# Performance work log

Measured on AMD Instinct MI355X. Metric: run time of the kernel, lower is better.

## Reference

```python
import jax, jax.numpy as jnp
import numpy as np

CHUNK = 32


def l2norm(x):
    return x * jax.lax.rsqrt(jnp.sum(x * x, -1, keepdims=True) + 1e-6)


def causal_dwconv(x, w):
    # x: (b, l, C), w: (C, 1, k) -- depthwise causal 1D conv (left pad k-1)
    k = w.shape[-1]
    xt = jnp.transpose(x, (0, 2, 1))
    xt = jnp.pad(xt, ((0, 0), (0, 0), (k - 1, 0)))
    y = jax.lax.conv_general_dilated(xt, w, (1,), 'VALID',
                                     dimension_numbers=('NCH', 'OIH', 'NCH'),
                                     feature_group_count=xt.shape[1])
    return jnp.transpose(y, (0, 2, 1))


def delta_rule_chunkwise(q, k, v, beta):
    # q,k: (b,h,L,dk), v: (b,h,L,dv), beta: (b,h,L). L must be divisible by CHUNK.
    b, h, L, dk = q.shape
    dv = v.shape[-1]
    n = L // CHUNK
    q = l2norm(q)
    k = l2norm(k)
    v = v * beta[..., None]
    kb = k * beta[..., None]
    resh = lambda t: t.reshape(b, h, n, CHUNK, t.shape[-1])
    q, k, v, kb = (resh(t) for t in (q, k, v, kb))
    strict = jnp.tril(jnp.ones((CHUNK, CHUNK), bool), -1)
    A = jnp.where(strict, -(kb @ jnp.swapaxes(k, -1, -2)), 0.0)
    eye = jnp.eye(CHUNK, dtype=A.dtype)
    # UT transform: the sequential forward-substitution loop computes T = (I - A)^{-1}
    T = jax.scipy.linalg.solve_triangular(eye - A, jnp.broadcast_to(eye, A.shape), lower=True)
    u = T @ v
    w = T @ kb
    incl = jnp.tril(jnp.ones((CHUNK, CHUNK), bool))  # lower incl. diag

    def step(S, xs):
        q_i, k_i, u_i, w_i = xs
        attn = jnp.where(incl, q_i @ jnp.swapaxes(k_i, -1, -2), 0.0)
        u_hat = u_i - w_i @ S
        o_i = q_i @ S + attn @ u_hat
        return S + jnp.swapaxes(k_i, -1, -2) @ u_hat, o_i

    xs = tuple(jnp.moveaxis(t, 2, 0) for t in (q, k, u, w))
    S0 = jnp.zeros((b, h, dk, dv), q.dtype)
    S, o = jax.lax.scan(step, S0, xs)
    o = jnp.moveaxis(o, 0, 2).reshape(b, h, L, dv)
    return o, S


def branch_stats(x):
    # per-head stats over the feature dim: mean, std(ddof=1), mean|x|, L2 norm
    m = jnp.mean(x, -1, keepdims=True)
    s = jnp.std(x, -1, keepdims=True, ddof=1)
    a = jnp.mean(jnp.abs(x), -1, keepdims=True)
    l = jnp.sqrt(jnp.sum(x * x, -1, keepdims=True))
    return jnp.concatenate([m, s, a, l], -1)


def reference(hidden_states, q_w, k_w, v_w, b_w, qc_w, kc_w, vc_w,
              fir_w1, fir_w3, fir_w7, fir_w31,
              mlp_w1, mlp_b1, mlp_w2, mlp_b2, gate_log_temp, onorm_w, o_w):
    B, L, D = hidden_states.shape
    H = gate_log_temp.shape[0]
    dk = q_w.shape[1] // H
    dv = v_w.shape[1] // H
    # projections + causal short conv + silu
    q = jax.nn.silu(causal_dwconv(hidden_states @ q_w, qc_w))
    k = jax.nn.silu(causal_dwconv(hidden_states @ k_w, kc_w))
    v = jax.nn.silu(causal_dwconv(hidden_states @ v_w, vc_w))
    q = q.reshape(B, L, H, dk)
    k = k.reshape(B, L, H, dk)
    v_direct = v.reshape(B, L, H, dv)
    beta = jax.nn.sigmoid(hidden_states @ b_w)  # (B,L,H)
    delta_out, _ = delta_rule_chunkwise(
        jnp.transpose(q, (0, 2, 1, 3)), jnp.transpose(k, (0, 2, 1, 3)),
        jnp.transpose(v_direct, (0, 2, 1, 3)), jnp.transpose(beta, (0, 2, 1)))
    delta_out = jnp.transpose(delta_out, (0, 2, 1, 3))  # (B,L,H,dv)
    # multi-scale depthwise FIR branches on v
    v_flat = v_direct.reshape(B, L, H * dv)
    firs = [causal_dwconv(v_flat, w).reshape(B, L, H, dv)
            for w in (fir_w1, fir_w3, fir_w7, fir_w31)]
    branches = firs + [delta_out, v_direct]  # num_streams = 6
    S = len(branches)
    stats = jnp.concatenate([branch_stats(x) for x in branches], -1)  # (B,L,H,S*4)
    gate_in = jnp.concatenate([hidden_states, stats.reshape(B, L, H * S * 4)], -1)
    hgate = jax.nn.gelu(gate_in @ mlp_w1 + mlp_b1, approximate=False)
    logits = (hgate @ mlp_w2 + mlp_b2).reshape(B, L, H, S)
    temp = jax.nn.softplus(gate_log_temp) + 0.5  # min_gate_temp = 0.5
    weights = jax.nn.softmax(logits / temp[None, None, :, None], axis=-1)
    fused = sum(weights[..., i, None] * br for i, br in enumerate(branches))
    # RMSNorm over head_v_dim (eps=1e-5)
    fused = fused * jax.lax.rsqrt(jnp.mean(fused * fused, -1, keepdims=True) + 1e-5) * onorm_w
    return fused.reshape(B, L, H * dv) @ o_w


def setup_inputs() -> dict:
    key = jax.random.key(0)
    B, L, D, H = 2, 2048, 1024, 4
    dk = dv = D // H
    S = 6
    ks = iter(jax.random.split(key, 32))
    nrm = lambda shape, s=0.02: jax.random.normal(next(ks), shape, jnp.float32) * s

    def fir(kw):
        # delta init (last tap = 1) plus small noise
        base = jnp.zeros((H * dv, 1, kw), jnp.float32).at[:, 0, -1].set(1.0)
        return base + nrm((H * dv, 1, kw))

    gate_in_dim = D + S * 4 * H  # 1120
    hgd = D * 2 // 2             # 1024
    b2 = np.zeros(H * S, np.float32)
    for h in range(H):
        b2[h * S + S - 1] = 2.0  # value_bias_init on direct-value stream
    return {
        'hidden_states': jax.random.normal(next(ks), (B, L, D), jnp.float32),
        'q_w': nrm((D, D)), 'k_w': nrm((D, D)), 'v_w': nrm((D, D)),
        'b_w': nrm((D, H)),
        'qc_w': nrm((D, 1, 4), 0.3), 'kc_w': nrm((D, 1, 4), 0.3), 'vc_w': nrm((D, 1, 4), 0.3),
        'fir_w1': fir(1), 'fir_w3': fir(3), 'fir_w7': fir(7), 'fir_w31': fir(31),
        'mlp_w1': nrm((gate_in_dim, hgd)), 'mlp_b1': jnp.zeros((hgd,), jnp.float32),
        'mlp_w2': nrm((hgd, H * S)), 'mlp_b2': jnp.asarray(b2),
        'gate_log_temp': jnp.zeros((H,), jnp.float32),
        'onorm_w': jnp.ones((dv,), jnp.float32),
        'o_w': nrm((D, D)),
    }
```

## Files before the change

kernel.cpp:

```cpp
#include <hip/hip_runtime.h>
#include <hip/hip_bf16.h>
#include <math.h>

#define B_ 2
#define L_ 2048
#define D_ 1024
#define H_ 4
#define NC 64

typedef unsigned short ushort_t;
typedef __bf16 bf16x8 __attribute__((ext_vector_type(8)));
typedef float f32x4 __attribute__((ext_vector_type(4)));
typedef ushort_t u16x8 __attribute__((ext_vector_type(8)));
typedef short s16x8 __attribute__((ext_vector_type(8)));
typedef short s16x4 __attribute__((ext_vector_type(4)));

__device__ __forceinline__ ushort_t f2bs(float f) {
    __hip_bfloat16 h = __float2bfloat16(f);
    ushort_t u;
    __builtin_memcpy(&u, &h, 2);
    return u;
}

__device__ __forceinline__ float wred(float v) {
    v += __shfl_down(v, 32);
    v += __shfl_down(v, 16);
    v += __shfl_down(v, 8);
    v += __shfl_down(v, 4);
    v += __shfl_down(v, 2);
    v += __shfl_down(v, 1);
    return v;
}

__device__ __forceinline__ void gload16(const void* g, void* l) {
    __builtin_amdgcn_global_load_lds((const __attribute__((address_space(1))) void*)g,
                                     (__attribute__((address_space(3))) void*)l, 16, 0, 0);
}

__device__ __forceinline__ s16x4 pack4(float a, float b, float c, float d) {
    ushort4 u;
    u.x = f2bs(a); u.y = f2bs(b); u.z = f2bs(c); u.w = f2bs(d);
    return __builtin_bit_cast(s16x4, u);
}
__device__ __forceinline__ bf16x8 cat8(s16x4 lo, s16x4 hi) {
    s16x8 r = __builtin_shufflevector(lo, hi, 0, 1, 2, 3, 4, 5, 6, 7);
    return __builtin_bit_cast(bf16x8, r);
}

__global__ __launch_bounds__(256) void tcast_k(const float* __restrict__ W,
                                               ushort_t* __restrict__ WT, int K, int N) {
    __shared__ float tile[32 * 33];
    const int k0 = blockIdx.y << 5, n0 = blockIdx.x << 5;
    for (int e = threadIdx.x; e < 1024; e += 256)
        tile[(e >> 5) * 33 + (e & 31)] = W[(size_t)(k0 + (e >> 5)) * N + n0 + (e & 31)];
    __syncthreads();
    for (int e = threadIdx.x; e < 1024; e += 256)
        WT[(size_t)(n0 + (e >> 5)) * K + k0 + (e & 31)] = f2bs(tile[(e & 31) * 33 + (e >> 5)]);
}

__global__ __launch_bounds__(256) void cast_k(const float* __restrict__ x,
                                              ushort_t* __restrict__ y) {
    const int i = blockIdx.x * 256 + threadIdx.x;
    const float4 v = *(const float4*)&x[(size_t)i * 4];
    ushort4 p;
    p.x = f2bs(v.x); p.y = f2bs(v.y); p.z = f2bs(v.z); p.w = f2bs(v.w);
    *(ushort4*)&y[(size_t)i * 4] = p;
}

template <int ACT>
__global__ __launch_bounds__(256) void gemm_bf(const ushort_t* __restrict__ A,
                                               const ushort_t* __restrict__ Bt,
                                               const float* __restrict__ bias,
                                               float* __restrict__ C,
                                               int M, int N, int K) {
    __shared__ ushort_t As[128 * 32];
    __shared__ ushort_t Bs[128 * 32];
    const int t = threadIdx.x;
    const int wv = t >> 6, l = t & 63;
    const int m0 = blockIdx.y << 7, n0 = blockIdx.x << 7;
    const int wm = wv & 1, wn = wv >> 1;
    const int q4 = l >> 4, c16 = l & 15;
    f32x4 acc[4][4];
#pragma unroll
    for (int i = 0; i < 4; ++i)
#pragma unroll
        for (int j = 0; j < 4; ++j) {
            f32x4 z = {0.f, 0.f, 0.f, 0.f};
            acc[i][j] = z;
        }
    const int srow = (l >> 2);
    const int scol = (l & 3) << 3;
    for (int k0 = 0; k0 < K; k0 += 32) {
        __syncthreads();
#pragma unroll
        for (int si = 0; si < 2; ++si) {
            const int s = wv * 2 + si;
            gload16(&A[(size_t)(m0 + s * 16 + srow) * K + k0 + scol], &As[s * 512]);
            gload16(&Bt[(size_t)(n0 + s * 16 + srow) * K + k0 + scol], &Bs[s * 512]);
        }
        __syncthreads();
        bf16x8 af[4], bff[4];
#pragma unroll
        for (int mi = 0; mi < 4; ++mi)
            af[mi] = *(const bf16x8*)&As[(wm * 64 + mi * 16 + c16) * 32 + q4 * 8];
#pragma unroll
        for (int ni = 0; ni < 4; ++ni)
            bff[ni] = *(const bf16x8*)&Bs[(wn * 64 + ni * 16 + c16) * 32 + q4 * 8];
#pragma unroll
        for (int mi = 0; mi < 4; ++mi)
#pragma unroll
            for (int ni = 0; ni < 4; ++ni)
                acc[mi][ni] = __builtin_amdgcn_mfma_f32_16x16x32_bf16(af[mi], bff[ni],
                                                                     acc[mi][ni], 0, 0, 0);
    }
#pragma unroll
    for (int mi = 0; mi < 4; ++mi)
#pragma unroll
        for (int ni = 0; ni < 4; ++ni)
#pragma unroll
            for (int r = 0; r < 4; ++r) {
                const int row = m0 + wm * 64 + mi * 16 + q4 * 4 + r;
                const int col = n0 + wn * 64 + ni * 16 + c16;
                float v = acc[mi][ni][r];
                if (ACT == 1) {
                    v += bias[col];
                    v = 0.5f * v * (1.0f + erff(v * 0.70710678118654752f));
                }
                C[(size_t)row * N + col] = v;
            }
}

template <int DO_NORM, int EMIT_F32, int EMIT_BF>
__global__ __launch_bounds__(256) void convql_k(const float* __restrict__ X,
                                                const float* __restrict__ cw,
                                                float* __restrict__ Y,
                                                ushort_t* __restrict__ Ybf) {
    __shared__ float xs[35 * 256];
    const int bid = blockIdx.x;
    const int h = bid & 3, lt = (bid >> 2) & 63, b = bid >> 8;
    const int t = threadIdx.x;
    const int l0 = lt << 5;
    const int cg = (h << 8) | t;
    for (int e = t; e < 35 * 256; e += 256) {
        const int r = e >> 8, c = e & 255;
        const int gl = l0 + r - 3;
        xs[e] = (gl >= 0) ? X[((size_t)(b * L_) + gl) * 3072 + (h << 8) + c] : 0.f;
    }
    const float w0 = cw[cg * 4 + 0], w1 = cw[cg * 4 + 1];
    const float w2 = cw[cg * 4 + 2], w3 = cw[cg * 4 + 3];
    __syncthreads();
    float yr[32];
#pragma unroll
    for (int l = 0; l < 32; ++l) {
        const float a = xs[(l + 0) * 256 + t] * w0 + xs[(l + 1) * 256 + t] * w1 +
                        xs[(l + 2) * 256 + t] * w2 + xs[(l + 3) * 256 + t] * w3;
        yr[l] = a / (1.f + expf(-a));
    }
    if (DO_NORM) {
        __syncthreads();
#pragma unroll
        for (int l = 0; l < 32; ++l) xs[l * 256 + t] = yr[l];
        __syncthreads();
        const int wv = t >> 6, lane = t & 63;
#pragma unroll
        for (int ri = 0; ri < 8; ++ri) {
            const int r = wv * 8 + ri;
            float4 v = *(float4*)&xs[r * 256 + lane * 4];
            float ss = v.x * v.x + v.y * v.y + v.z * v.z + v.w * v.w;
            ss = wred(ss);
            ss = __shfl(ss, 0);
            const float s = rsqrtf(ss + 1e-6f);
            v.x *= s; v.y *= s; v.z *= s; v.w *= s;
            const size_t go = ((size_t)(b * L_) + l0 + r) * 1024 + (h << 8) + lane * 4;
            if (EMIT_F32) *(float4*)&Y[go] = v;
            if (EMIT_BF) {
                ushort4 p;
                p.x = f2bs(v.x); p.y = f2bs(v.y); p.z = f2bs(v.z); p.w = f2bs(v.w);
                *(ushort4*)&Ybf[go] = p;
            }
        }
    } else {
#pragma unroll
        for (int l = 0; l < 32; ++l)
            if (EMIT_F32) Y[((size_t)(b * L_) + l0 + l) * 1024 + cg] = yr[l];
    }
}

__global__ __launch_bounds__(256) void fir_k(const float* __restrict__ V,
                                             const float* __restrict__ w1w,
                                             const float* __restrict__ w3w,
                                             const float* __restrict__ w7w,
                                             const float* __restrict__ w31w,
                                             float* __restrict__ o1,
                                             float* __restrict__ o3,
                                             float* __restrict__ o7,
                                             float* __restrict__ o31) {
    __shared__ float xs[62 * 256];
    const int bid = blockIdx.x;
    const int h = bid & 3, lt = (bid >> 2) & 63, b = bid >> 8;
    const int t = threadIdx.x;
    const int l0 = lt << 5;
    const int cg = (h << 8) | t;
    for (int e = t; e < 62 * 256; e += 256) {
        const int r = e >> 8, c = e & 255;
        const int gl = l0 + r - 30;
        xs[e] = (gl >= 0) ? V[((size_t)(b * L_) + gl) * 1024 + (h << 8) + c] : 0.f;
    }
    float lw31[31], lw7[7], lw3[3];
#pragma unroll
    for (int j = 0; j < 31; ++j) lw31[j] = w31w[cg * 31 + j];
#pragma unroll
    for (int j = 0; j < 7; ++j) lw7[j] = w7w[cg * 7 + j];
#pragma unroll
    for (int j = 0; j < 3; ++j) lw3[j] = w3w[cg * 3 + j];
    const float lw1 = w1w[cg];
    __syncthreads();
    for (int l = 0; l < 32; ++l) {
        float a31 = 0.f, a7 = 0.f, a3 = 0.f, v = 0.f;
#pragma unroll
        for (int j = 0; j < 31; ++j) {
            v = xs[(l + j) * 256 + t];
            a31 += v * lw31[j];
            if (j >= 24) a7 += v * lw7[j - 24];
            if (j >= 28) a3 += v * lw3[j - 28];
        }
        const size_t go = ((size_t)(b * L_) + l0 + l) * 1024 + cg;
        o31[go] = a31;
        o7[go] = a7;
        o3[go] = a3;
        o1[go] = v * lw1;
    }
}

__global__ __launch_bounds__(64) void beta_k(const float* __restrict__ hs,
                                             const float* __restrict__ bw,
                                             float* __restrict__ beta,
                                             ushort_t* __restrict__ gin) {
    const int row = blockIdx.x;
    const int lane = threadIdx.x;
    float a0 = 0, a1 = 0, a2 = 0, a3 = 0;
    const float* hp = hs + (size_t)row * D_;
    ushort_t* gp = gin + (size_t)row * 1120;
    for (int c = lane; c < D_; c += 64) {
        const float x = hp[c];
        gp[c] = f2bs(x);
        a0 += x * bw[c * 4 + 0];
        a1 += x * bw[c * 4 + 1];
        a2 += x * bw[c * 4 + 2];
        a3 += x * bw[c * 4 + 3];
    }
    a0 = wred(a0); a1 = wred(a1); a2 = wred(a2); a3 = wred(a3);
    if (lane == 0) {
        float* o = beta + (size_t)row * 4;
        o[0] = 1.f / (1.f + expf(-a0));
        o[1] = 1.f / (1.f + expf(-a1));
        o[2] = 1.f / (1.f + expf(-a2));
        o[3] = 1.f / (1.f + expf(-a3));
    }
}

__global__ __launch_bounds__(256) void prep2_k(const ushort_t* __restrict__ qbf,
                                               const ushort_t* __restrict__ kbf,
                                               const float* __restrict__ vg,
                                               const float* __restrict__ beta,
                                               ushort_t* __restrict__ qfr,
                                               ushort_t* __restrict__ wfr,
                                               float* __restrict__ ufr,
                                               ushort_t* __restrict__ atfr,
                                               ushort_t* __restrict__ ktfr) {
    __shared__ ushort_t k_lds[32 * 264];
    __shared__ ushort_t kT_lds[256 * 32];
    __shared__ ushort_t vT_lds[256 * 32];
    __shared__ float Am[32 * 33];
    __shared__ float Tm[32 * 33];
    __shared__ ushort_t Tb[32 * 40];
    __shared__ ushort_t at_s[32 * 40];
    __shared__ float beta_s[32];
    const int bid = blockIdx.x;
    const int bh = bid >> 6, ci = bid & 63;
    const int b = bh >> 2, h = bh & 3;
    const int t = threadIdx.x;
    const int wv = t >> 6, lane = t & 63;
    const int mi = wv & 1, ni = wv >> 1;
    const int l16 = lane & 15, quad = lane >> 4;
    const size_t cb = (size_t)bid;
    const size_t grow = ((size_t)(b * L_ + ci * 32)) * 1024 + (h << 8);
    const f32x4 z4 = {0.f, 0.f, 0.f, 0.f};

    if (t < 32) beta_s[t] = beta[(size_t)(b * L_ + ci * 32 + t) * 4 + h];
#pragma unroll
    for (int j = 0; j < 4; ++j) {
        const int idx = j * 2048 + t * 8, r = idx >> 8, c = idx & 255;
        *(u16x8*)&k_lds[r * 264 + c] = *(const u16x8*)&kbf[grow + (size_t)r * 1024 + c];
    }
#pragma unroll
    for (int j = 0; j < 8; ++j) {
        const int e = j * 1024 + t * 4, r = e >> 8, c = e & 255;
        const float4 v4 = *(const float4*)&vg[grow + (size_t)r * 1024 + c];
        const float vv[4] = {v4.x, v4.y, v4.z, v4.w};
#pragma unroll
        for (int x = 0; x < 4; ++x) {
            const int cc = c + x;
            const int sp = (r >> 3) ^ ((cc >> 1) & 3);
            vT_lds[cc * 32 + sp * 8 + (r & 7)] = f2bs(vv[x]);
        }
    }
    f32x4 g = z4, atv = z4;
#pragma unroll
    for (int s = 0; s < 8; ++s) {
        const bf16x8 a =
            *(const bf16x8*)&kbf[grow + (size_t)(mi * 16 + l16) * 1024 + s * 32 + (quad << 3)];
        const bf16x8 bb =
            *(const bf16x8*)&kbf[grow + (size_t)(ni * 16 + l16) * 1024 + s * 32 + (quad << 3)];
        const bf16x8 qa =
            *(const bf16x8*)&qbf[grow + (size_t)(mi * 16 + l16) * 1024 + s * 32 + (quad << 3)];
        g = __builtin_amdgcn_mfma_f32_16x16x32_bf16(a, bb, g, 0, 0, 0);
        atv = __builtin_amdgcn_mfma_f32_16x16x32_bf16(qa, bb, atv, 0, 0, 0);
        if (ni == 0) {
            const size_t ga = grow + (size_t)(mi * 16 + l16) * 1024 + s * 32 + (quad << 2);
            const ushort4 q0 = *(const ushort4*)&qbf[ga];
            const ushort4 q1 = *(const ushort4*)&qbf[ga + 16];
            ushort_t* qd = &qfr[((cb * 2 + mi) * 8 + s) * 512 + lane * 8];
            *(ushort4*)qd = q0;
            *(ushort4*)(qd + 4) = q1;
        }
    }
    __syncthreads();
#pragma unroll
    for (int r = 0; r < 4; ++r) {
        const int row = mi * 16 + (quad << 2) + r;
        const int col = ni * 16 + l16;
        Am[row * 33 + col] = (col < row) ? -beta_s[row] * g[r] : 0.f;
        Tm[row * 33 + col] = (row == col) ? 1.f : 0.f;
        at_s[row * 40 + col] = (col <= row) ? f2bs(atv[r]) : (ushort_t)0;
    }
#pragma unroll
    for (int j = 0; j < 8; ++j) {
        const int e = j * 1024 + t * 4, r = e >> 8, c = e & 255;
#pragma unroll
        for (int x = 0; x < 4; ++x) {
            const int cc = c + x;
            const int sp = (r >> 3) ^ ((cc >> 1) & 3);
            kT_lds[cc * 32 + sp * 8 + (r & 7)] = k_lds[r * 264 + cc];
        }
    }
    __syncthreads();
    if (wv < 2) {
        const int ra = (wv * 16 + l16) * 40 + (quad << 2);
        const ushort4 a0 = *(const ushort4*)&at_s[ra];
        const ushort4 a1 = *(const ushort4*)&at_s[ra + 16];
        ushort_t* ad = &atfr[(cb * 2 + wv) * 512 + lane * 8];
        *(ushort4*)ad = a0;
        *(ushort4*)(ad + 4) = a1;
    }
#pragma unroll
    for (int j2 = 0; j2 < 4; ++j2) {
        const int tc = wv * 4 + j2;
        const int d = tc * 16 + l16;
        const int x = (d >> 1) & 3;
        const int base = d * 32 + ((quad & 1) << 2);
        const ushort4 k0 = *(const ushort4*)&kT_lds[base + ((((quad >> 1) + 0) ^ x) << 3)];
        const ushort4 k1 = *(const ushort4*)&kT_lds[base + ((((quad >> 1) + 2) ^ x) << 3)];
        ushort_t* kd = &ktfr[(cb * 16 + tc) * 512 + lane * 8];
        *(ushort4*)kd = k0;
        *(ushort4*)(kd + 4) = k1;
    }
    for (int i = 1; i < 32; ++i) {
        if (t < 32) {
            float s = 0.f;
            for (int j = 0; j < i; ++j) s += Am[i * 33 + j] * Tm[j * 33 + t];
            Tm[i * 33 + t] += s;
        }
        __syncthreads();
    }
#pragma unroll
    for (int j = 0; j < 4; ++j) {
        const int e = j * 256 + t, i = e >> 5, jj = e & 31;
        Tb[i * 40 + jj] = f2bs(Tm[i * 33 + jj] * beta_s[jj]);
    }
    __syncthreads();
    const bf16x8 tf = *(const bf16x8*)&Tb[(mi * 16 + l16) * 40 + (quad << 3)];
#pragma unroll
    for (int j = 0; j < 8; ++j) {
        const int nt = ni * 8 + j;
        const int d = (nt << 4) + l16;
        const int sp = quad ^ ((d >> 1) & 3);
        const bf16x8 kb = *(const bf16x8*)&kT_lds[d * 32 + (sp << 3)];
        const bf16x8 vb = *(const bf16x8*)&vT_lds[d * 32 + (sp << 3)];
        const f32x4 wacc = __builtin_amdgcn_mfma_f32_16x16x32_bf16(tf, kb, z4, 0, 0, 0);
        const f32x4 uacc = __builtin_amdgcn_mfma_f32_16x16x32_bf16(tf, vb, z4, 0, 0, 0);
        *(float4*)&ufr[((cb * 16 + nt) * 2 + mi) * 256 + lane * 4] =
            make_float4(uacc[0], uacc[1], uacc[2], uacc[3]);
#pragma unroll
        for (int r = 0; r < 4; ++r) {
            const int row = mi * 16 + (quad << 2) + r;
            k_lds[row * 264 + d] = f2bs(wacc[r]);
        }
    }
    __syncthreads();
    if (wv < 2) {
#pragma unroll
        for (int sp = 0; sp < 8; ++sp) {
            const int rb = (wv * 16 + l16) * 264 + sp * 32 + (quad << 2);
            const ushort4 w0 = *(const ushort4*)&k_lds[rb];
            const ushort4 w1 = *(const ushort4*)&k_lds[rb + 16];
            ushort_t* wd = &wfr[((cb * 2 + wv) * 8 + sp) * 512 + lane * 8];
            *(ushort4*)wd = w0;
            *(ushort4*)(wd + 4) = w1;
        }
    }
}

__global__ __launch_bounds__(64, 1) void scan10_k(const ushort_t* __restrict__ qfr,
                                                  const ushort_t* __restrict__ wfr,
                                                  const float* __restrict__ ufr,
                                                  const ushort_t* __restrict__ atfr,
                                                  const ushort_t* __restrict__ ktfr,
                                                  float* __restrict__ dlt) {
    __shared__ ushort_t qstg[2][16 * 512];
    __shared__ ushort_t wstg[2][16 * 512];
    __shared__ ushort_t ktstg[2][16 * 512];
    __shared__ ushort_t atstg[2][2 * 512];
    __shared__ float ustg[2][4 * 256];
    const int l = threadIdx.x;
    const int qd = l >> 4, c = l & 15;
    const int bh = blockIdx.x & 7, pair = blockIdx.x >> 3;
    const int t0 = pair * 2;
    const int b = bh >> 2, h = bh & 3;

    f32x4 Sacc[2][16];
    s16x4 SB[2][16];
#pragma unroll
    for (int tt = 0; tt < 2; ++tt)
#pragma unroll
        for (int tc = 0; tc < 16; ++tc) {
            f32x4 z = {0.f, 0.f, 0.f, 0.f};
            Sacc[tt][tc] = z;
            s16x4 zs = {0, 0, 0, 0};
            SB[tt][tc] = zs;
        }

    auto stage = [&](int ci, int p) {
        const size_t cb = (size_t)(bh * NC + ci);
        const ushort_t* qsrc = qfr + cb * (16 * 512);
        const ushort_t* wsrc = wfr + cb * (16 * 512);
        const ushort_t* ksrc = ktfr + cb * (16 * 512);
#pragma unroll
        for (int f = 0; f < 16; ++f) gload16(&qsrc[f * 512 + l * 8], &qstg[p][f * 512]);
#pragma unroll
        for (int f = 0; f < 16; ++f) gload16(&wsrc[f * 512 + l * 8], &wstg[p][f * 512]);
#pragma unroll
        for (int f = 0; f < 16; ++f) gload16(&ksrc[f * 512 + l * 8], &ktstg[p][f * 512]);
#pragma unroll
        for (int hf = 0; hf < 2; ++hf)
            gload16(&atfr[(cb * 2 + hf) * 512 + l * 8], &atstg[p][hf * 512]);
#pragma unroll
        for (int tt = 0; tt < 2; ++tt)
#pragma unroll
            for (int hf = 0; hf < 2; ++hf)
                gload16(&ufr[((cb * 16 + t0 + tt) * 2 + hf) * 256 + l * 4],
                        &ustg[p][(tt * 2 + hf) * 256]);
    };

    stage(0, 0);
    asm volatile("s_waitcnt vmcnt(0)" ::: "memory");
    __builtin_amdgcn_sched_barrier(0);

    for (int ci = 0; ci < NC; ++ci) {
        const int p = ci & 1;
        asm volatile("s_waitcnt vmcnt(8)" ::: "memory");
        __builtin_amdgcn_sched_barrier(0);
        if (ci + 1 < NC) stage(ci + 1, p ^ 1);

        f32x4 aw[2][2], oq[2][2];
#pragma unroll
        for (int tt = 0; tt < 2; ++tt)
#pragma unroll
            for (int hf = 0; hf < 2; ++hf) {
                f32x4 z = {0.f, 0.f, 0.f, 0.f};
                aw[tt][hf] = z;
                oq[tt][hf] = z;
            }
#pragma unroll
        for (int sp = 0; sp < 8; ++sp) {
            bf16x8 Sop[2];
#pragma unroll
            for (int tt = 0; tt < 2; ++tt)
                Sop[tt] = cat8(SB[tt][2 * sp + 0], SB[tt][2 * sp + 1]);
#pragma unroll
            for (int hf = 0; hf < 2; ++hf) {
                const bf16x8 wv8 = *(const bf16x8*)&wstg[p][(hf * 8 + sp) * 512 + l * 8];
                const bf16x8 qv8 = *(const bf16x8*)&qstg[p][(hf * 8 + sp) * 512 + l * 8];
#pragma unroll
                for (int tt = 0; tt < 2; ++tt) {
                    aw[tt][hf] =
                        __builtin_amdgcn_mfma_f32_16x16x32_bf16(wv8, Sop[tt], aw[tt][hf], 0, 0, 0);
                    oq[tt][hf] =
                        __builtin_amdgcn_mfma_f32_16x16x32_bf16(qv8, Sop[tt], oq[tt][hf], 0, 0, 0);
                }
            }
        }
        bf16x8 Uop[2];
#pragma unroll
        for (int tt = 0; tt < 2; ++tt) {
            s16x4 uhB[2];
#pragma unroll
            for (int hf = 0; hf < 2; ++hf) {
                const float4 uv = *(const float4*)&ustg[p][(tt * 2 + hf) * 256 + l * 4];
                uhB[hf] = pack4(uv.x - aw[tt][hf][0], uv.y - aw[tt][hf][1],
                                uv.z - aw[tt][hf][2], uv.w - aw[tt][hf][3]);
            }
            Uop[tt] = cat8(uhB[0], uhB[1]);
        }
#pragma unroll
        for (int tc = 0; tc < 16; ++tc) {
            const bf16x8 ktv = *(const bf16x8*)&ktstg[p][tc * 512 + l * 8];
#pragma unroll
            for (int tt = 0; tt < 2; ++tt) {
                Sacc[tt][tc] = __builtin_amdgcn_mfma_f32_16x16x32_bf16(ktv, Uop[tt],
                                                                       Sacc[tt][tc], 0, 0, 0);
                SB[tt][tc] = pack4(Sacc[tt][tc][0], Sacc[tt][tc][1], Sacc[tt][tc][2],
                                   Sacc[tt][tc][3]);
            }
        }
#pragma unroll
        for (int hf = 0; hf < 2; ++hf) {
            const bf16x8 av = *(const bf16x8*)&atstg[p][hf * 512 + l * 8];
#pragma unroll
            for (int tt = 0; tt < 2; ++tt)
                oq[tt][hf] =
                    __builtin_amdgcn_mfma_f32_16x16x32_bf16(av, Uop[tt], oq[tt][hf], 0, 0, 0);
        }
        const size_t gb0 = ((size_t)(b * L_ + ci * 32)) * 1024 + (h << 8) + c;
#pragma unroll
        for (int tt = 0; tt < 2; ++tt)
#pragma unroll
            for (int hf = 0; hf < 2; ++hf)
#pragma unroll
                for (int r = 0; r < 4; ++r)
                    dlt[gb0 + ((t0 + tt) << 4) + (size_t)(hf * 16 + (qd << 2) + r) * 1024] =
                        oq[tt][hf][r];
    }
}

__global__ __launch_bounds__(64) void stats_k(const float* __restrict__ f1,
                                              const float* __restrict__ f3,
                                              const float* __restrict__ f7,
                                              const float* __restrict__ f31,
                                              const float* __restrict__ dl,
                                              const float* __restrict__ vv,
                                              ushort_t* __restrict__ gin) {
    const int row = blockIdx.x;
    const int lane = threadIdx.x;
    const float* ptrs[6] = {f1, f3, f7, f31, dl, vv};
    const size_t base = (size_t)row * 256;
    ushort_t* gp = gin + (size_t)(row >> 2) * 1120 + 1024 + (row & 3) * 24;
    for (int br = 0; br < 6; ++br) {
        const float4 x = *(const float4*)&ptrs[br][base + lane * 4];
        float s1 = x.x + x.y + x.z + x.w;
        float s2 = x.x * x.x + x.y * x.y + x.z * x.z + x.w * x.w;
        float sa = fabsf(x.x) + fabsf(x.y) + fabsf(x.z) + fabsf(x.w);
        s1 = wred(s1); s2 = wred(s2); sa = wred(sa);
        if (lane == 0) {
            const float m = s1 / 256.f;
            float var = (s2 - 256.f * m * m) / 255.f;
            if (var < 0.f) var = 0.f;
            gp[br * 4 + 0] = f2bs(m);
            gp[br * 4 + 1] = f2bs(sqrtf(var));
            gp[br * 4 + 2] = f2bs(sa / 256.f);
            gp[br * 4 + 3] = f2bs(sqrtf(s2));
        }
    }
}

__global__ __launch_bounds__(256) void wts_k(const float* __restrict__ hg,
                                             const float* __restrict__ w2,
                                             const float* __restrict__ b2,
                                             const float* __restrict__ glt,
                                             float* __restrict__ wts) {
    const int row = blockIdx.x;
    const int h = threadIdx.x >> 6, lane = threadIdx.x & 63;
    float hv[16];
    const float* hp = hg + (size_t)row * 1024;
#pragma unroll
    for (int ii = 0; ii < 16; ++ii) hv[ii] = hp[lane + 64 * ii];
    float lg[6];
#pragma unroll
    for (int s = 0; s < 6; ++s) {
        const int j = h * 6 + s;
        float acc = 0.f;
#pragma unroll
        for (int ii = 0; ii < 16; ++ii) acc += hv[ii] * w2[(size_t)(lane + 64 * ii) * 24 + j];
        lg[s] = wred(acc);
    }
    if (lane == 0) {
        const float temp = log1pf(expf(glt[h])) + 0.5f;
        float mx = -1e30f;
#pragma unroll
        for (int s = 0; s < 6; ++s) {
            lg[s] = (lg[s] + b2[h * 6 + s]) / temp;
            mx = fmaxf(mx, lg[s]);
        }
        float se = 0.f;
#pragma unroll
        for (int s = 0; s < 6; ++s) {
            lg[s] = expf(lg[s] - mx);
            se += lg[s];
        }
        float* o = &wts[(size_t)row * 24 + h * 6];
        const float inv = 1.f / se;
#pragma unroll
        for (int s = 0; s < 6; ++s) o[s] = lg[s] * inv;
    }
}

__global__ __launch_bounds__(1024) void fuse_k(const float* __restrict__ f1,
                                               const float* __restrict__ f3,
                                               const float* __restrict__ f7,
                                               const float* __restrict__ f31,
                                               const float* __restrict__ dl,
                                               const float* __restrict__ vv,
                                               const float* __restrict__ wts,
                                               const float* __restrict__ onw,
                                               ushort_t* __restrict__ fused) {
    __shared__ float wloc[24];
    __shared__ float psum[16];
    const int row = blockIdx.x, t = threadIdx.x;
    if (t < 24) wloc[t] = wts[(size_t)row * 24 + t];
    __syncthreads();
    const int h = t >> 8, dd = t & 255;
    const size_t idx = (size_t)row * 1024 + t;
    const float* ptrs[6] = {f1, f3, f7, f31, dl, vv};
    float f = 0.f;
#pragma unroll
    for (int br = 0; br < 6; ++br) f += wloc[h * 6 + br] * ptrs[br][idx];
    float ss = wred(f * f);
    const int wave = t >> 6;
    if ((t & 63) == 0) psum[wave] = ss;
    __syncthreads();
    const float tot = psum[h * 4 + 0] + psum[h * 4 + 1] + psum[h * 4 + 2] + psum[h * 4 + 3];
    const float scale = rsqrtf(tot / 256.f + 1e-5f);
    fused[idx] = f2bs(f * scale * onw[dd]);
}

extern "C" void kernel_launch(void* const* d_in, const int* in_sizes, int n_in,
                              void* d_out, int out_size, void* d_ws, size_t ws_size,
                              hipStream_t stream) {
    const float* hs   = (const float*)d_in[0];
    const float* q_w  = (const float*)d_in[1];
    const float* k_w  = (const float*)d_in[2];
    const float* v_w  = (const float*)d_in[3];
    const float* b_w  = (const float*)d_in[4];
    const float* qc_w = (const float*)d_in[5];
    const float* kc_w = (const float*)d_in[6];
    const float* vc_w = (const float*)d_in[7];
    const float* f1w  = (const float*)d_in[8];
    const float* f3w  = (const float*)d_in[9];
    const float* f7w  = (const float*)d_in[10];
    const float* f31w = (const float*)d_in[11];
    const float* w1   = (const float*)d_in[12];
    const float* b1   = (const float*)d_in[13];
    const float* w2   = (const float*)d_in[14];
    const float* b2   = (const float*)d_in[15];
    const float* glt  = (const float*)d_in[16];
    const float* onw  = (const float*)d_in[17];
    const float* o_w  = (const float*)d_in[18];
    float* out = (float*)d_out;

    const size_t SZ = (size_t)B_ * L_ * D_;
    float* qlin = (float*)d_ws;
    float* klin = qlin + SZ;
    float* vlin = klin + SZ;
    float* qbuf = vlin + SZ;
    float* kbuf = qbuf + SZ;
    float* vbuf = kbuf + SZ;
    float* f31b = vbuf + SZ;
    float* wb   = f31b + SZ;
    float* ub   = wb + SZ;
    float* dlt  = ub + SZ;
    float* beta = dlt + SZ;
    float* attn = beta + (size_t)B_ * L_ * H_;
    float* f1b = qlin;
    float* f3b = klin;
    float* f7b = vlin;
    float* hgate = kbuf;
    float* qkv = qlin;
    float* wts = attn + (size_t)B_ * H_ * NC * 1024;

    ushort_t* hs_bf = (ushort_t*)dlt;
    ushort_t* qwT = (ushort_t*)f31b;
    ushort_t* kwT = (ushort_t*)f31b + 1048576;
    ushort_t* vwT = (ushort_t*)f31b + 2097152;
    ushort_t* qbf = (ushort_t*)f31b + 3145728;
    ushort_t* kbf = (ushort_t*)kbuf;
    ushort_t* gin_bf = (ushort_t*)qbuf;
    ushort_t* w1T = (ushort_t*)(wb + 2359296);
    ushort_t* owT = (ushort_t*)ub;
    ushort_t* fused_bf = (ushort_t*)kbuf;
    ushort_t* ktfr = (ushort_t*)klin;
    ushort_t* qfr = (ushort_t*)klin + SZ;
    ushort_t* wfr = (ushort_t*)wb;
    float* ufr = ub;
    ushort_t* atfr = (ushort_t*)attn;

    const int M = B_ * L_;

    tcast_k<<<dim3(32, 32), 256, 0, stream>>>(q_w, qwT, 1024, 1024);
    tcast_k<<<dim3(32, 32), 256, 0, stream>>>(k_w, kwT, 1024, 1024);
    tcast_k<<<dim3(32, 32), 256, 0, stream>>>(v_w, vwT, 1024, 1024);
    cast_k<<<4096, 256, 0, stream>>>(hs, hs_bf);
    gemm_bf<0><<<dim3(24, 32), 256, 0, stream>>>(hs_bf, qwT, nullptr, qkv, M, 3072, 1024);
    beta_k<<<M, 64, 0, stream>>>(hs, b_w, beta, gin_bf);
    convql_k<1, 0, 1><<<512, 256, 0, stream>>>(qkv + 0,    qc_w, nullptr, qbf);
    convql_k<1, 0, 1><<<512, 256, 0, stream>>>(qkv + 1024, kc_w, nullptr, kbf);
    convql_k<0, 1, 0><<<512, 256, 0, stream>>>(qkv + 2048, vc_w, vbuf, nullptr);
    prep2_k<<<B_ * H_ * NC, 256, 0, stream>>>(qbf, kbf, vbuf, beta, qfr, wfr, ufr, atfr, ktfr);
    scan10_k<<<64, 64, 0, stream>>>(qfr, wfr, ufr, atfr, ktfr, dlt);
    fir_k<<<512, 256, 0, stream>>>(vbuf, f1w, f3w, f7w, f31w, f1b, f3b, f7b, f31b);
    stats_k<<<M * H_, 64, 0, stream>>>(f1b, f3b, f7b, f31b, dlt, vbuf, gin_bf);
    tcast_k<<<dim3(32, 35), 256, 0, stream>>>(w1, w1T, 1120, 1024);
    gemm_bf<1><<<dim3(8, 32), 256, 0, stream>>>(gin_bf, w1T, b1, hgate, M, 1024, 1120);
    wts_k<<<M, 256, 0, stream>>>(hgate, w2, b2, glt, wts);
    fuse_k<<<M, 1024, 0, stream>>>(f1b, f3b, f7b, f31b, dlt, vbuf, wts, onw, fused_bf);
    tcast_k<<<dim3(32, 32), 256, 0, stream>>>(o_w, owT, 1024, 1024);
    gemm_bf<0><<<dim3(8, 32), 256, 0, stream>>>(fused_bf, owT, nullptr, out, M, 1024, 1024);
}
```

Baseline: 649.9 us.

## Split scan across one value tile per block and preload LDS operands to registers

The recurrent scan kernel now assigns a single 16-column value tile per workgroup instead of two, doubling the grid from 64 to 128 single-wave blocks so more CUs work on the sequential chunk recurrence. Each block holds half the state accumulators, shortening the per-chunk MFMA dependency chain. All LDS fragments for a chunk are also loaded into registers up front to overlap LDS latency with MFMA work. The cost is that q, w, k and attention tiles are staged redundantly by twice as many blocks, doubling that global/LDS traffic, and register pressure rises from the preloads.

```diff
diff --git a/kernel.cpp b/kernel.cpp
--- a/kernel.cpp
+++ b/kernel.cpp
@@ -411,7 +411,7 @@
     }
 }
 
-__global__ __launch_bounds__(64, 1) void scan10_k(const ushort_t* __restrict__ qfr,
+__global__ __launch_bounds__(64, 1) void scan11_k(const ushort_t* __restrict__ qfr,
                                                   const ushort_t* __restrict__ wfr,
                                                   const float* __restrict__ ufr,
                                                   const ushort_t* __restrict__ atfr,
@@ -421,24 +421,21 @@
     __shared__ ushort_t wstg[2][16 * 512];
     __shared__ ushort_t ktstg[2][16 * 512];
     __shared__ ushort_t atstg[2][2 * 512];
-    __shared__ float ustg[2][4 * 256];
+    __shared__ float ustg[2][2 * 256];
     const int l = threadIdx.x;
     const int qd = l >> 4, c = l & 15;
-    const int bh = blockIdx.x & 7, pair = blockIdx.x >> 3;
-    const int t0 = pair * 2;
+    const int bh = blockIdx.x & 7, tile = blockIdx.x >> 3;
     const int b = bh >> 2, h = bh & 3;
 
-    f32x4 Sacc[2][16];
-    s16x4 SB[2][16];
-#pragma unroll
-    for (int tt = 0; tt < 2; ++tt)
-#pragma unroll
-        for (int tc = 0; tc < 16; ++tc) {
-            f32x4 z = {0.f, 0.f, 0.f, 0.f};
-            Sacc[tt][tc] = z;
-            s16x4 zs = {0, 0, 0, 0};
-            SB[tt][tc] = zs;
-        }
+    f32x4 Sacc[16];
+    s16x4 SB[16];
+#pragma unroll
+    for (int tc = 0; tc < 16; ++tc) {
+        f32x4 z = {0.f, 0.f, 0.f, 0.f};
+        Sacc[tc] = z;
+        s16x4 zs = {0, 0, 0, 0};
+        SB[tc] = zs;
+    }
 
     auto stage = [&](int ci, int p) {
         const size_t cb = (size_t)(bh * NC + ci);
@@ -455,11 +452,8 @@
         for (int hf = 0; hf < 2; ++hf)
             gload16(&atfr[(cb * 2 + hf) * 512 + l * 8], &atstg[p][hf * 512]);
 #pragma unroll
-        for (int tt = 0; tt < 2; ++tt)
-#pragma unroll
-            for (int hf = 0; hf < 2; ++hf)
-                gload16(&ufr[((cb * 16 + t0 + tt) * 2 + hf) * 256 + l * 4],
-                        &ustg[p][(tt * 2 + hf) * 256]);
+        for (int hf = 0; hf < 2; ++hf)
+            gload16(&ufr[((cb * 16 + tile) * 2 + hf) * 256 + l * 4], &ustg[p][hf * 256]);
     };
 
     stage(0, 0);
@@ -472,74 +466,61 @@
         __builtin_amdgcn_sched_barrier(0);
         if (ci + 1 < NC) stage(ci + 1, p ^ 1);
 
-        f32x4 aw[2][2], oq[2][2];
-#pragma unroll
-        for (int tt = 0; tt < 2; ++tt)
+        bf16x8 wr[16], qr[16], ktr[16], atr[2];
+        float4 ur[2];
+#pragma unroll
+        for (int f = 0; f < 16; ++f) {
+            wr[f] = *(const bf16x8*)&wstg[p][f * 512 + l * 8];
+            qr[f] = *(const bf16x8*)&qstg[p][f * 512 + l * 8];
+            ktr[f] = *(const bf16x8*)&ktstg[p][f * 512 + l * 8];
+        }
+#pragma unroll
+        for (int hf = 0; hf < 2; ++hf) {
+            atr[hf] = *(const bf16x8*)&atstg[p][hf * 512 + l * 8];
+            ur[hf] = *(const float4*)&ustg[p][hf * 256 + l * 4];
+        }
+
+        f32x4 aw[2], oq[2];
+#pragma unroll
+        for (int hf = 0; hf < 2; ++hf) {
+            f32x4 z = {0.f, 0.f, 0.f, 0.f};
+            aw[hf] = z;
+            oq[hf] = z;
+        }
+#pragma unroll
+        for (int sp = 0; sp < 8; ++sp) {
+            const bf16x8 Sop = cat8(SB[2 * sp + 0], SB[2 * sp + 1]);
 #pragma unroll
             for (int hf = 0; hf < 2; ++hf) {
-                f32x4 z = {0.f, 0.f, 0.f, 0.f};
-                aw[tt][hf] = z;
-                oq[tt][hf] = z;
+                aw[hf] = __builtin_amdgcn_mfma_f32_16x16x32_bf16(wr[hf * 8 + sp], Sop,
+                                                                 aw[hf], 0, 0, 0);
+                oq[hf] = __builtin_amdgcn_mfma_f32_16x16x32_bf16(qr[hf * 8 + sp], Sop,
+                                                                 oq[hf], 0, 0, 0);
             }
-#pragma unroll
-        for (int sp = 0; sp < 8; ++sp) {
-            bf16x8 Sop[2];
-#pragma unroll
-            for (int tt = 0; tt < 2; ++tt)
-                Sop[tt] = cat8(SB[tt][2 * sp + 0], SB[tt][2 * sp + 1]);
-#pragma unroll
-            for (int hf = 0; hf < 2; ++hf) {
-                const bf16x8 wv8 = *(const bf16x8*)&wstg[p][(hf * 8 + sp) * 512 + l * 8];
-                const bf16x8 qv8 = *(const bf16x8*)&qstg[p][(hf * 8 + sp) * 512 + l * 8];
-#pragma unroll
-                for (int tt = 0; tt < 2; ++tt) {
-                    aw[tt][hf] =
-                        __builtin_amdgcn_mfma_f32_16x16x32_bf16(wv8, Sop[tt], aw[tt][hf], 0, 0, 0);
-                    oq[tt][hf] =
-                        __builtin_amdgcn_mfma_f32_16x16x32_bf16(qv8, Sop[tt], oq[tt][hf], 0, 0, 0);
-                }
-            }
-        }
-        bf16x8 Uop[2];
-#pragma unroll
-        for (int tt = 0; tt < 2; ++tt) {
-            s16x4 uhB[2];
-#pragma unroll
-            for (int hf = 0; hf < 2; ++hf) {
-                const float4 uv = *(const float4*)&ustg[p][(tt * 2 + hf) * 256 + l * 4];
-                uhB[hf] = pack4(uv.x - aw[tt][hf][0], uv.y - aw[tt][hf][1],
-                                uv.z - aw[tt][hf][2], uv.w - aw[tt][hf][3]);
-            }
-            Uop[tt] = cat8(uhB[0], uhB[1]);
-        }
+        }
+        s16x4 uhB[2];
+#pragma unroll
+        for (int hf = 0; hf < 2; ++hf) {
+            const float4 uv = ur[hf];
+            uhB[hf] = pack4(uv.x - aw[hf][0], uv.y - aw[hf][1],
+                            uv.z - aw[hf][2], uv.w - aw[hf][3]);
+        }
+        const bf16x8 Uop = cat8(uhB[0], uhB[1]);
 #pragma unroll
         for (int tc = 0; tc < 16; ++tc) {
-            const bf16x8 ktv = *(const bf16x8*)&ktstg[p][tc * 512 + l * 8];
-#pragma unroll
-            for (int tt = 0; tt < 2; ++tt) {
-                Sacc[tt][tc] = __builtin_amdgcn_mfma_f32_16x16x32_bf16(ktv, Uop[tt],
-                                                                       Sacc[tt][tc], 0, 0, 0);
-                SB[tt][tc] = pack4(Sacc[tt][tc][0], Sacc[tt][tc][1], Sacc[tt][tc][2],
-                                   Sacc[tt][tc][3]);
-            }
-        }
-#pragma unroll
-        for (int hf = 0; hf < 2; ++hf) {
-            const bf16x8 av = *(const bf16x8*)&atstg[p][hf * 512 + l * 8];
-#pragma unroll
-            for (int tt = 0; tt < 2; ++tt)
-                oq[tt][hf] =
-                    __builtin_amdgcn_mfma_f32_16x16x32_bf16(av, Uop[tt], oq[tt][hf], 0, 0, 0);
-        }
-        const size_t gb0 = ((size_t)(b * L_ + ci * 32)) * 1024 + (h << 8) + c;
-#pragma unroll
-        for (int tt = 0; tt < 2; ++tt)
-#pragma unroll
-            for (int hf = 0; hf < 2; ++hf)
-#pragma unroll
-                for (int r = 0; r < 4; ++r)
-                    dlt[gb0 + ((t0 + tt) << 4) + (size_t)(hf * 16 + (qd << 2) + r) * 1024] =
-                        oq[tt][hf][r];
+            Sacc[tc] = __builtin_amdgcn_mfma_f32_16x16x32_bf16(ktr[tc], Uop, Sacc[tc], 0, 0, 0);
+            SB[tc] = pack4(Sacc[tc][0], Sacc[tc][1], Sacc[tc][2], Sacc[tc][3]);
+        }
+#pragma unroll
+        for (int hf = 0; hf < 2; ++hf)
+            oq[hf] = __builtin_amdgcn_mfma_f32_16x16x32_bf16(atr[hf], Uop, oq[hf], 0, 0, 0);
+        const size_t gbase =
+            ((size_t)(b * L_ + ci * 32)) * 1024 + (h << 8) + (tile << 4) + c;
+#pragma unroll
+        for (int hf = 0; hf < 2; ++hf)
+#pragma unroll
+            for (int r = 0; r < 4; ++r)
+                dlt[gbase + (size_t)(hf * 16 + (qd << 2) + r) * 1024] = oq[hf][r];
     }
 }
 
@@ -715,7 +696,7 @@
     convql_k<1, 0, 1><<<512, 256, 0, stream>>>(qkv + 1024, kc_w, nullptr, kbf);
     convql_k<0, 1, 0><<<512, 256, 0, stream>>>(qkv + 2048, vc_w, vbuf, nullptr);
     prep2_k<<<B_ * H_ * NC, 256, 0, stream>>>(qbf, kbf, vbuf, beta, qfr, wfr, ufr, atfr, ktfr);
-    scan10_k<<<64, 64, 0, stream>>>(qfr, wfr, ufr, atfr, ktfr, dlt);
+    scan11_k<<<128, 64, 0, stream>>>(qfr, wfr, ufr, atfr, ktfr, dlt);
     fir_k<<<512, 256, 0, stream>>>(vbuf, f1w, f3w, f7w, f31w, f1b, f3b, f7b, f31b);
     stats_k<<<M * H_, 64, 0, stream>>>(f1b, f3b, f7b, f31b, dlt, vbuf, gin_bf);
     tcast_k<<<dim3(32, 35), 256, 0, stream>>>(w1, w1T, 1120, 1024);
```

Result: faster. 610.5 us (-6.1%).
